# Kernel optimization log

Measured on AMD Instinct MI355X. Metric: run time of the kernel, lower is better.

## Reference

```python
import jax, jax.numpy as jnp
import numpy as np

R_EPS = 1e-15

def _sdf_net(x, W1, b1, W2, b2):
    h = jax.nn.relu(x @ W1 + b1)
    return h @ W2 + b2  # [..., 1+feat]

def _fd_gradient(x, W1, b1, W2, b2, eps):
    # central finite differences of the SDF along the 3 axes
    offs = eps * jnp.eye(3, dtype=x.dtype)              # [3,3]
    xp = x[None, :, :] + offs[:, None, :]               # [3,P,3]
    xm = x[None, :, :] - offs[:, None, :]
    sp = _sdf_net(xp, W1, b1, W2, b2)[..., 0]           # [3,P]
    sm = _sdf_net(xm, W1, b1, W2, b2)[..., 0]
    return ((sp - sm) / (2.0 * eps)).T                  # [P,3]

def _softplus100(x):
    # torch.nn.Softplus(beta=100)
    return jax.nn.softplus(100.0 * x) / 100.0

def _exclusive_cumprod(a):
    ones = jnp.ones_like(a[:, :1])
    return jnp.cumprod(jnp.concatenate([ones, a], -1), -1)[:, :-1]

def _sample_pdf(bins, weights, n_samples):
    # bins [R,K], weights [R,K-1]; deterministic inverse-CDF sampling (det=True)
    weights = weights + 1e-5
    pdf = weights / jnp.sum(weights, -1, keepdims=True)
    cdf = jnp.cumsum(pdf, -1)
    cdf = jnp.concatenate([jnp.zeros_like(cdf[:, :1]), cdf], -1)  # [R,K]
    K = cdf.shape[-1]
    u = jnp.linspace(0.5 / n_samples, 1.0 - 0.5 / n_samples, n_samples, dtype=bins.dtype)
    u = jnp.broadcast_to(u[None], (bins.shape[0], n_samples))
    inds = jax.vmap(lambda c, uu: jnp.searchsorted(c, uu, side='right'))(cdf, u)
    below = jnp.clip(inds - 1, 0, K - 1)
    above = jnp.clip(inds, 0, K - 1)
    cdf_b = jnp.take_along_axis(cdf, below, -1)
    cdf_a = jnp.take_along_axis(cdf, above, -1)
    bin_b = jnp.take_along_axis(bins, below, -1)
    bin_a = jnp.take_along_axis(bins, above, -1)
    denom = cdf_a - cdf_b
    denom = jnp.where(denom < 1e-5, jnp.ones_like(denom), denom)
    t = (u - cdf_b) / denom
    return bin_b + t * (bin_a - bin_b)

def _forward(rays_o, rays_d, W1, b1, W2, b2, Wc1, bc1, Wc2, bc2, inv_s_param,
             num_steps, upsample_steps, bound):
    B, N = rays_o.shape[:2]
    ro = rays_o.reshape(-1, 3)
    rd = rays_d.reshape(-1, 3)
    R = ro.shape[0]
    bnd = float(bound)
    # near/far from cube bound
    tmin = (-bnd - ro) / (rd + R_EPS)
    tmax = (bnd - ro) / (rd + R_EPS)
    near = jnp.max(jnp.minimum(tmin, tmax), -1, keepdims=True)
    far = jnp.min(jnp.maximum(tmin, tmax), -1, keepdims=True)
    near = jnp.maximum(near, 0.05)
    z = jnp.linspace(0.0, 1.0, num_steps, dtype=ro.dtype)[None]
    z_vals = near + (far - near) * z                     # [R,S0]
    sample_dist = (far - near) / num_steps               # [R,1]
    pts = ro[:, None, :] + rd[:, None, :] * z_vals[..., None]
    pts = jnp.clip(pts, -bnd, bnd)
    # --- coarse SDF pass + inverse-CDF importance resampling (torch.no_grad) ---
    sdf_c = _sdf_net(pts.reshape(-1, 3), W1, b1, W2, b2)[:, 0].reshape(R, num_steps)
    sdf_c = jax.lax.stop_gradient(sdf_c)
    d_c = z_vals[:, 1:] - z_vals[:, :-1]
    mid_sdf = 0.5 * (sdf_c[:, 1:] + sdf_c[:, :-1])
    cos_val = jnp.clip((sdf_c[:, 1:] - sdf_c[:, :-1]) / (d_c + 1e-5), -1e3, 0.0)
    prev_c = jax.nn.sigmoid((mid_sdf - cos_val * d_c * 0.5) * 64.0)
    next_c = jax.nn.sigmoid((mid_sdf + cos_val * d_c * 0.5) * 64.0)
    alpha_c = jnp.clip((prev_c - next_c + 1e-5) / (prev_c + 1e-5), 0.0, 1.0)
    w_c = alpha_c * _exclusive_cumprod(1.0 - alpha_c + 1e-7)
    new_z = jax.lax.stop_gradient(_sample_pdf(z_vals, w_c, upsample_steps))
    z_vals = jnp.sort(jnp.concatenate([z_vals, new_z], -1), -1)
    S = num_steps + upsample_steps
    # --- fine pass: deltas / midpoints / shading / NeuS compositing ---
    deltas = z_vals[:, 1:] - z_vals[:, :-1]
    deltas = jnp.concatenate([deltas, jnp.broadcast_to(sample_dist, (R, 1))], -1)
    z_mid = jnp.concatenate([z_vals[:, :-1] + 0.5 * deltas[:, :-1], z_vals[:, -1:]], -1)
    new_pts = ro[:, None, :] + rd[:, None, :] * z_mid[..., None]
    new_pts = jnp.clip(new_pts, -bnd, bnd)
    flat_pts = new_pts.reshape(-1, 3)                    # [R*S,3]
    out = _sdf_net(flat_pts, W1, b1, W2, b2)
    sdf = out[:, :1]
    feat = out[:, 1:]
    grad = _fd_gradient(flat_pts, W1, b1, W2, b2, 0.005)  # eps=0.005*(1-ratio), ratio=0
    normal = grad / (1e-5 + jnp.linalg.norm(grad, axis=-1, keepdims=True))
    dirs = jnp.broadcast_to(rd[:, None, :], new_pts.shape).reshape(-1, 3)
    cin = jnp.concatenate([flat_pts, dirs, normal, feat], -1)
    color = jax.nn.sigmoid(jax.nn.relu(cin @ Wc1 + bc1) @ Wc2 + bc2)   # [R*S,3]
    inv_s = jnp.exp(10.0 * inv_s_param)                   # forward_variance()
    true_cos = jnp.sum(dirs * normal, -1, keepdims=True)
    iter_cos = -_softplus100(-true_cos)                   # cos_anneal_ratio = 1.0
    d_flat = deltas.reshape(-1, 1)
    prev_cdf = jax.nn.sigmoid((sdf - iter_cos * d_flat * 0.5) * inv_s)
    next_cdf = jax.nn.sigmoid((sdf + iter_cos * d_flat * 0.5) * inv_s)
    alpha = jnp.clip((prev_cdf - next_cdf + 1e-5) / (prev_cdf + 1e-5), 0.0, 1.0).reshape(R, S)
    weights = alpha * _exclusive_cumprod(1.0 - alpha + 1e-7)
    weights_sum = jnp.sum(weights, -1, keepdims=True)
    image = jnp.sum(color.reshape(R, S, 3) * weights[..., None], 1)
    image = image + (1.0 - weights_sum) * 1.0             # bg_color = 1
    return image.reshape(B, N, 3)

def setup_inputs() -> dict:
    key = jax.random.key(0)
    ks = jax.random.split(key, 8)
    B, N, H, F = 1, 4096, 64, 64
    rays_o = (jax.random.uniform(ks[0], (B, N, 3), jnp.float32) - 0.5) * 0.5
    d = jax.random.normal(ks[1], (B, N, 3), jnp.float32)
    rays_d = d / (1e-8 + jnp.linalg.norm(d, axis=-1, keepdims=True))
    def lin(k, i, o):
        return jax.random.normal(k, (i, o), jnp.float32) / np.sqrt(i).astype(np.float32)
    W1 = lin(ks[2], 3, H); b1 = jnp.zeros((H,), jnp.float32)
    W2 = lin(ks[3], H, 1 + F); b2 = jnp.zeros((1 + F,), jnp.float32)
    Wc1 = lin(ks[4], 9 + F, H); bc1 = jnp.zeros((H,), jnp.float32)
    Wc2 = lin(ks[5], H, 3); bc2 = jnp.zeros((3,), jnp.float32)
    inv_s_param = jnp.full((1,), 0.3, jnp.float32)
    return {"rays_o": rays_o, "rays_d": rays_d, "W1": W1, "b1": b1, "W2": W2, "b2": b2,
            "Wc1": Wc1, "bc1": bc1, "Wc2": Wc2, "bc2": bc2, "inv_s_param": inv_s_param,
            "num_steps": 64, "upsample_steps": 64, "bound": 1}

def reference(rays_o, rays_d, W1, b1, W2, b2, Wc1, bc1, Wc2, bc2, inv_s_param,
              num_steps, upsample_steps, bound):
    return _forward(rays_o, rays_d, W1, b1, W2, b2, Wc1, bc1, Wc2, bc2, inv_s_param,
                    num_steps, upsample_steps, bound)
```

## Files before the change

### kernel.cpp

```cpp
#include <hip/hip_runtime.h>
#include <hip/hip_bf16.h>
#include <cmath>

#define KS 84

#define OFF_W1    0
#define OFF_W1E   256
#define OFF_W1S   512
#define OFF_WC2   768
#define OFF_BC2   1024
#define OFF_GC    1028
#define OFF_AF    1032

typedef __attribute__((ext_vector_type(4))) short  short4v;
typedef __attribute__((ext_vector_type(8))) short  short8v;
typedef __attribute__((ext_vector_type(16))) float f32x16;

__device__ __forceinline__ float sigm(float x){ return 1.0f/(1.0f + expf(-x)); }
__device__ __forceinline__ float clampf(float x, float lo, float hi){ return fminf(fmaxf(x, lo), hi); }
__device__ __forceinline__ unsigned short f2bf(float x){
  __hip_bfloat16 h = __float2bfloat16(x);
  return *reinterpret_cast<unsigned short*>(&h);
}
__device__ __forceinline__ unsigned pk2(float a, float b){
  return (unsigned)f2bf(a) | ((unsigned)f2bf(b) << 16);
}
__device__ __forceinline__ unsigned cvt_pk_bf16(float a, float b){
  unsigned r;
  asm("v_cvt_pk_bf16_f32 %0, %1, %2" : "=v"(r) : "v"(a), "v"(b));
  return r;
}
__device__ __forceinline__ short8v lds_load8(const unsigned short* p){
  short4v lo = *(const short4v*)p;
  short4v hi = *(const short4v*)(p + 4);
  short8v r;
  r[0]=lo[0]; r[1]=lo[1]; r[2]=lo[2]; r[3]=lo[3];
  r[4]=hi[0]; r[5]=hi[1]; r[6]=hi[2]; r[7]=hi[3];
  return r;
}

__global__ __launch_bounds__(256)
void prep_weights(const float* __restrict__ W1, const float* __restrict__ b1,
                  const float* __restrict__ W2, const float* __restrict__ b2,
                  const float* __restrict__ Wc1, const float* __restrict__ bc1,
                  const float* __restrict__ Wc2, const float* __restrict__ bc2,
                  float* __restrict__ ws)
{
  __shared__ float LW2[4160];
  __shared__ float LWc1[4672];
  __shared__ float LW1[192];
  __shared__ float Lb1[64];
  __shared__ float Lb2[65];
  __shared__ float Lbc1[64];
  __shared__ float LWc2[192];
  __shared__ float Lbc2[3];
  __shared__ float s_cb[4][64];
  __shared__ unsigned short W2T[64*KS];
  __shared__ unsigned short ABUF[64*KS];
  const int tid  = threadIdx.x;
  const int lane = tid & 63;
  const int wv   = tid >> 6;
  const int l31  = lane & 31;
  const int h    = lane >> 5;

  {
    const float4* s4 = (const float4*)W2;
    float4* d4 = (float4*)LW2;
    for (int i = tid; i < 1040; i += 256) d4[i] = s4[i];
    const float4* c4 = (const float4*)Wc1;
    float4* e4 = (float4*)LWc1;
    for (int i = tid; i < 1168; i += 256) e4[i] = c4[i];
  }
  if (tid < 192) LW1[tid]  = W1[tid];
  if (tid < 64)  Lb1[tid]  = b1[tid];
  if (tid < 65)  Lb2[tid]  = b2[tid];
  if (tid < 64)  Lbc1[tid] = bc1[tid];
  if (tid < 192) LWc2[tid] = Wc2[tid];
  if (tid < 3)   Lbc2[tid] = bc2[tid];
  __syncthreads();

  for (int i = tid; i < 4096; i += 256){
    int k = i >> 6, t = i & 63;
    W2T[k*KS + t] = f2bf(LW2[k*65 + 1 + t]);
  }
  for (int i = tid; i < 576; i += 256){
    int ii = i >> 6, c = i & 63;
    ABUF[c*KS + 64 + ii] = f2bf(LWc1[ii*64 + c]);
  }
  for (int i = tid; i < 384; i += 256){
    int z = i >> 6, c = i & 63;
    ABUF[c*KS + 74 + z] = 0;
  }
  {
    int c = tid & 63, q = tid >> 6;
    float acc = 0.f;
    #pragma unroll
    for (int t = 16*q; t < 16*q + 16; ++t)
      acc = fmaf(Lb2[1+t], LWc1[(9+t)*64 + c], acc);
    s_cb[q][c] = acc;
  }
  if (tid < 64){
    int j = tid;
    float wx = LW1[j], wy = LW1[64+j], wz = LW1[128+j];
    float w2 = LW2[j*65];
    float Hx = 0.005f * fabsf(wx);
    float Hy = 0.005f * fabsf(wy);
    float Hz = 0.005f * fabsf(wz);
    float Sx = (wx < 0.f) ? -w2 : w2;
    float Sy = (wy < 0.f) ? -w2 : w2;
    float Sz = (wz < 0.f) ? -w2 : w2;
    ws[OFF_W1 + 4*j + 0] = wx;
    ws[OFF_W1 + 4*j + 1] = wy;
    ws[OFF_W1 + 4*j + 2] = wz;
    ws[OFF_W1 + 4*j + 3] = Lb1[j];
    ws[OFF_W1E + 4*j + 0] = Hx;
    ws[OFF_W1E + 4*j + 1] = Hy;
    ws[OFF_W1E + 4*j + 2] = Hz;
    ws[OFF_W1E + 4*j + 3] = w2;
    ws[OFF_W1S + 4*j + 0] = Sx;
    ws[OFF_W1S + 4*j + 1] = Sy;
    ws[OFF_W1S + 4*j + 2] = Sz;
    ws[OFF_W1S + 4*j + 3] = 0.f;
    float sx = Sx*Hx, sy = Sy*Hy, sz = Sz*Hz;
    #pragma unroll
    for (int off = 1; off < 64; off <<= 1){
      sx += __shfl_xor(sx, off);
      sy += __shfl_xor(sy, off);
      sz += __shfl_xor(sz, off);
    }
    if (j == 0){
      ws[OFF_GC + 0] = sx;
      ws[OFF_GC + 1] = sy;
      ws[OFF_GC + 2] = sz;
    }
  } else if (tid < 128){
    int j = tid - 64;
    ws[OFF_WC2 + 4*j + 0] = LWc2[j*3+0];
    ws[OFF_WC2 + 4*j + 1] = LWc2[j*3+1];
    ws[OFF_WC2 + 4*j + 2] = LWc2[j*3+2];
    ws[OFF_WC2 + 4*j + 3] = 0.f;
  } else if (tid < 132){
    int j = tid - 128;
    ws[OFF_BC2 + j] = (j < 3) ? Lbc2[j] : Lb2[0];
  }
  __syncthreads();

  if (tid < 64){
    float acc = Lbc1[tid] + ((s_cb[0][tid] + s_cb[1][tid]) + (s_cb[2][tid] + s_cb[3][tid]));
    ABUF[tid*KS + 73] = f2bf(acc);
  }
  {
    const int mb = wv & 1, kb = wv >> 1;
    f32x16 e;
    #pragma unroll
    for (int i = 0; i < 16; ++i) e[i] = 0.f;
    #pragma unroll
    for (int s = 0; s < 4; ++s){
      short8v afr;
      #pragma unroll
      for (int j = 0; j < 8; ++j)
        afr[j] = (short)f2bf(LWc1[(9 + 16*s + 8*h + j)*64 + 32*mb + l31]);
      short8v bfr = lds_load8(&W2T[(32*kb + l31)*KS + 16*s + 8*h]);
      e = __builtin_amdgcn_mfma_f32_32x32x16_bf16(afr, bfr, e, 0, 0, 0);
    }
    const int kcol = 32*kb + l31;
    #pragma unroll
    for (int r = 0; r < 16; ++r){
      int c = 32*mb + (r & 3) + 8*(r >> 2) + 4*h;
      ABUF[c*KS + kcol] = f2bf(e[r]);
    }
  }
  __syncthreads();

  for (int i = tid; i < 640; i += 256){
    int f = i >> 6, ln = i & 63;
    int mb = f / 5, kk = f - 5*mb;
    int c  = 32*mb + (ln & 31);
    int kb2 = 16*kk + 8*(ln >> 5);
    short8v v = lds_load8(&ABUF[c*KS + kb2]);
    *((short8v*)(((unsigned short*)(ws + OFF_AF)) + (size_t)i * 8)) = v;
  }
}

__global__ __launch_bounds__(128, 3)
void neus_render(const float* __restrict__ rays_o, const float* __restrict__ rays_d,
                 const float* __restrict__ inv_s_p, const float* __restrict__ ws,
                 float* __restrict__ out)
{
  __shared__ unsigned short s_aext[2][64*KS];
  __shared__ float4 s_wc2[64];
  __shared__ float  s_z[64];
  __shared__ float  s_cdf[64];
  __shared__ float  s_newz[64];
  __shared__ float  s_zall[128];
  __shared__ float  s_red[2][4];
  __shared__ float  s_wtot[2];

  const int tid  = threadIdx.x;
  const int lt   = tid;
  const int lane = tid & 63;
  const int wir  = tid >> 6;
  const int ray  = blockIdx.x;

  const float4* __restrict__ pW1  = (const float4*)(ws + OFF_W1);
  const float4* __restrict__ pW1E = (const float4*)(ws + OFF_W1E);
  const float4* __restrict__ pW1S = (const float4*)(ws + OFF_W1S);
  const float*  __restrict__ pbc2 = ws + OFF_BC2;
  const float*  __restrict__ pgc  = ws + OFF_GC;
  const float b20 = pbc2[3];

  if (tid < 64) s_wc2[tid] = ((const float4*)(ws + OFF_WC2))[tid];

  float ox = rays_o[ray*3], oy = rays_o[ray*3+1], oz = rays_o[ray*3+2];
  float dx = rays_d[ray*3], dy = rays_d[ray*3+1], dz = rays_d[ray*3+2];
  float tnx = (-1.f-ox)/(dx+1e-15f), tfx = (1.f-ox)/(dx+1e-15f);
  float tny = (-1.f-oy)/(dy+1e-15f), tfy = (1.f-oy)/(dy+1e-15f);
  float tnz = (-1.f-oz)/(dz+1e-15f), tfz = (1.f-oz)/(dz+1e-15f);
  float nearv = fmaxf(fmaxf(fminf(tnx,tfx), fminf(tny,tfy)), fminf(tnz,tfz));
  float farv  = fminf(fminf(fmaxf(tnx,tfx), fmaxf(tny,tfy)), fmaxf(tnz,tfz));
  nearv = fmaxf(nearv, 0.05f);
  const float sd = (farv - nearv) * (1.f/64.f);

  if (wir == 0){
    float zt = nearv + (farv-nearv) * ((float)lane * (1.f/63.f));
    float px = clampf(ox + dx*zt, -1.f, 1.f);
    float py = clampf(oy + dy*zt, -1.f, 1.f);
    float pz = clampf(oz + dz*zt, -1.f, 1.f);
    float acc0 = b20, acc1 = 0.f;
    #pragma unroll 4
    for (int q = 0; q < 32; ++q){
      int j = 2*q;
      float4 wa = pW1[j];
      float4 wb = pW1[j+1];
      float ea = pW1E[j].w;
      float eb = pW1E[j+1].w;
      float ha = fmaxf(fmaf(px, wa.x, fmaf(py, wa.y, fmaf(pz, wa.z, wa.w))), 0.f);
      float hb = fmaxf(fmaf(px, wb.x, fmaf(py, wb.y, fmaf(pz, wb.z, wb.w))), 0.f);
      acc0 = fmaf(ha, ea, acc0);
      acc1 = fmaf(hb, eb, acc1);
    }
    float acc = acc0 + acc1;
    s_z[lane] = zt;
    float s1  = __shfl_down(acc, 1);
    float zt1 = nearv + (farv-nearv) * ((float)(lane+1) * (1.f/63.f));
    float a_c = 0.f, qv = 1.f;
    if (lane < 63){
      float dc   = zt1 - zt;
      float mid  = 0.5f*(acc + s1);
      float cosv = clampf((s1-acc)/(dc+1e-5f), -1000.f, 0.f);
      float est  = cosv*dc*0.5f;
      float pcv  = sigm((mid-est)*64.f);
      float ncv  = sigm((mid+est)*64.f);
      a_c = clampf((pcv-ncv+1e-5f)/(pcv+1e-5f), 0.f, 1.f);
      qv  = 1.f - a_c + 1e-7f;
    }
    float p = qv;
    #pragma unroll
    for (int off = 1; off < 64; off <<= 1){
      float t = __shfl_up(p, off);
      if (lane >= off) p *= t;
    }
    float ec = __shfl_up(p, 1);
    if (lane == 0) ec = 1.f;
    float wvv = (lane < 63) ? (a_c*ec + 1e-5f) : 0.f;
    float tot = wvv;
    #pragma unroll
    for (int off = 32; off > 0; off >>= 1) tot += __shfl_xor(tot, off);
    float cs = wvv;
    #pragma unroll
    for (int off = 1; off < 64; off <<= 1){
      float t = __shfl_up(cs, off);
      if (lane >= off) cs += t;
    }
    if (lane == 0)  s_cdf[0] = 0.f;
    if (lane < 63)  s_cdf[lane+1] = cs / tot;
  }
  __syncthreads();

  if (wir == 0){
    float u = ((float)lane + 0.5f) * (1.f/64.f);
    int lo = 0, hi = 64;
    while (lo < hi){
      int m = (lo+hi) >> 1;
      if (s_cdf[m] <= u) lo = m+1; else hi = m;
    }
    int below = lo - 1;
    int above = lo < 63 ? lo : 63;
    float cb = s_cdf[below], ca = s_cdf[above];
    float bb = s_z[below],   ba = s_z[above];
    float den = ca - cb; if (den < 1e-5f) den = 1.f;
    float tt = (u - cb)/den;
    s_newz[lane] = bb + tt*(ba - bb);
  }
  __syncthreads();

  const short8v* pAF = (const short8v*)(ws + OFF_AF);
  short8v af[10];
  #pragma unroll
  for (int f = 0; f < 10; ++f) af[f] = pAF[f*64 + lane];

  {
    float v; int pos;
    if (lt < 64){
      v = s_z[lt];
      int lo = 0, hi = 64;
      while (lo < hi){ int m=(lo+hi)>>1; if (s_newz[m] < v) lo = m+1; else hi = m; }
      pos = lt + lo;
    } else {
      int jj = lt - 64;
      v = s_newz[jj];
      int lo = 0, hi = 64;
      while (lo < hi){ int m=(lo+hi)>>1; if (s_z[m] <= v) lo = m+1; else hi = m; }
      pos = jj + lo;
    }
    s_zall[pos] = v;
  }
  __syncthreads();

  float zc = s_zall[lt];
  float zn = s_zall[lt < 127 ? lt+1 : 127];
  float delta = (lt < 127) ? (zn - zc) : sd;
  float zm    = (lt < 127) ? (zc + 0.5f*delta) : zc;
  float px = clampf(ox + dx*zm, -1.f, 1.f);
  float py = clampf(oy + dy*zm, -1.f, 1.f);
  float pz = clampf(oz + dz*zm, -1.f, 1.f);

  unsigned short* arow = &s_aext[wir][(unsigned)lane * KS];
  float sa0 = b20, sa1 = 0.f;
  float gxa = pgc[0], gya = pgc[1], gza = pgc[2];
  float gxb = 0.f, gyb = 0.f, gzb = 0.f;
  #pragma unroll 2
  for (int q = 0; q < 16; ++q){
    int j = 4*q;
    float4 w0 = pW1[j],   e0 = pW1E[j],   s0 = pW1S[j];
    float4 w1 = pW1[j+1], e1 = pW1E[j+1], s1v = pW1S[j+1];
    float4 w2 = pW1[j+2], e2 = pW1E[j+2], s2v = pW1S[j+2];
    float4 w3 = pW1[j+3], e3 = pW1E[j+3], s3v = pW1S[j+3];
    float base0 = fmaf(px, w0.x, fmaf(py, w0.y, fmaf(pz, w0.z, w0.w)));
    float base1 = fmaf(px, w1.x, fmaf(py, w1.y, fmaf(pz, w1.z, w1.w)));
    float base2 = fmaf(px, w2.x, fmaf(py, w2.y, fmaf(pz, w2.z, w2.w)));
    float base3 = fmaf(px, w3.x, fmaf(py, w3.y, fmaf(pz, w3.z, w3.w)));
    float hv0 = fmaxf(base0, 0.f), hv1 = fmaxf(base1, 0.f);
    float hv2 = fmaxf(base2, 0.f), hv3 = fmaxf(base3, 0.f);
    sa0 = fmaf(hv0, e0.w, sa0); sa0 = fmaf(hv1, e1.w, sa0);
    sa1 = fmaf(hv2, e2.w, sa1); sa1 = fmaf(hv3, e3.w, sa1);
    gxa = fmaf(__builtin_amdgcn_fmed3f(base0, -e0.x, e0.x), s0.x, gxa);
    gya = fmaf(__builtin_amdgcn_fmed3f(base0, -e0.y, e0.y), s0.y, gya);
    gza = fmaf(__builtin_amdgcn_fmed3f(base0, -e0.z, e0.z), s0.z, gza);
    gxa = fmaf(__builtin_amdgcn_fmed3f(base1, -e1.x, e1.x), s1v.x, gxa);
    gya = fmaf(__builtin_amdgcn_fmed3f(base1, -e1.y, e1.y), s1v.y, gya);
    gza = fmaf(__builtin_amdgcn_fmed3f(base1, -e1.z, e1.z), s1v.z, gza);
    gxb = fmaf(__builtin_amdgcn_fmed3f(base2, -e2.x, e2.x), s2v.x, gxb);
    gyb = fmaf(__builtin_amdgcn_fmed3f(base2, -e2.y, e2.y), s2v.y, gyb);
    gzb = fmaf(__builtin_amdgcn_fmed3f(base2, -e2.z, e2.z), s2v.z, gzb);
    gxb = fmaf(__builtin_amdgcn_fmed3f(base3, -e3.x, e3.x), s3v.x, gxb);
    gyb = fmaf(__builtin_amdgcn_fmed3f(base3, -e3.y, e3.y), s3v.y, gyb);
    gzb = fmaf(__builtin_amdgcn_fmed3f(base3, -e3.z, e3.z), s3v.z, gzb);
    *(unsigned*)&arow[j]   = cvt_pk_bf16(hv0, hv1);
    *(unsigned*)&arow[j+2] = cvt_pk_bf16(hv2, hv3);
  }
  float sdfv = sa0 + sa1;
  float gx = (gxa+gxb)*100.f, gy = (gya+gyb)*100.f, gz = (gza+gzb)*100.f;
  float gn = 1e-5f + sqrtf(gx*gx + gy*gy + gz*gz);
  float nx = gx/gn, ny = gy/gn, nz = gz/gn;

  *(unsigned*)&arow[64] = cvt_pk_bf16(px, py);
  *(unsigned*)&arow[66] = cvt_pk_bf16(pz, dx);
  *(unsigned*)&arow[68] = cvt_pk_bf16(dy, dz);
  *(unsigned*)&arow[70] = cvt_pk_bf16(nx, ny);
  *(unsigned*)&arow[72] = cvt_pk_bf16(nz, 1.0f);
  *(unsigned*)&arow[74] = 0u;
  *(unsigned*)&arow[76] = 0u;
  *(unsigned*)&arow[78] = 0u;

  const float inv_s = expf(10.f * inv_s_p[0]);
  float tcos = dx*nx + dy*ny + dz*nz;
  float aarg = -100.f * tcos;
  float spv  = (aarg > 0.f) ? (aarg + log1pf(expf(-aarg))) : log1pf(expf(aarg));
  float iter_cos = -(spv * 0.01f);
  float est = iter_cos * delta * 0.5f;
  float pcv = sigm((sdfv - est)*inv_s);
  float ncv = sigm((sdfv + est)*inv_s);
  float alpha = clampf((pcv - ncv + 1e-5f)/(pcv + 1e-5f), 0.f, 1.f);

  float qv = 1.f - alpha + 1e-7f;
  float p = qv;
  #pragma unroll
  for (int off = 1; off < 64; off <<= 1){
    float t = __shfl_up(p, off);
    if (lane >= off) p *= t;
  }
  if (lane == 63) s_wtot[wir] = p;
  __syncthreads();
  float excl = __shfl_up(p, 1);
  if (lane == 0) excl = 1.f;
  if (wir == 1) excl *= s_wtot[0];
  float w  = alpha * excl;

  f32x16 acc00, acc01, acc10, acc11;
  #pragma unroll
  for (int i = 0; i < 16; ++i){ acc00[i]=0.f; acc01[i]=0.f; acc10[i]=0.f; acc11[i]=0.f; }
  const unsigned short* aw = s_aext[wir];
  const int scol = lane & 31;
  const int half8 = (lane >> 5) * 8;
  #pragma unroll
  for (int kk = 0; kk < 5; ++kk){
    int koff = 16*kk + half8;
    short8v b0 = lds_load8(&aw[ scol      * KS + koff]);
    short8v b1 = lds_load8(&aw[(32+scol) * KS + koff]);
    acc00 = __builtin_amdgcn_mfma_f32_32x32x16_bf16(af[kk],   b0, acc00, 0, 0, 0);
    acc10 = __builtin_amdgcn_mfma_f32_32x32x16_bf16(af[5+kk], b0, acc10, 0, 0, 0);
    acc01 = __builtin_amdgcn_mfma_f32_32x32x16_bf16(af[kk],   b1, acc01, 0, 0, 0);
    acc11 = __builtin_amdgcn_mfma_f32_32x32x16_bf16(af[5+kk], b1, acc11, 0, 0, 0);
  }

  float pr0=0.f,pr1=0.f,pr2=0.f,pr3=0.f,pr4=0.f,pr5=0.f;
  const int halfoff = (lane >> 5) * 4;
  #pragma unroll
  for (int r = 0; r < 16; ++r){
    int ci = (r & 3) + 8*(r >> 2) + halfoff;
    float4 wA = s_wc2[ci];
    float4 wB = s_wc2[32 + ci];
    float v;
    v = fmaxf(acc00[r], 0.f); pr0 = fmaf(v, wA.x, pr0); pr1 = fmaf(v, wA.y, pr1); pr2 = fmaf(v, wA.z, pr2);
    v = fmaxf(acc10[r], 0.f); pr0 = fmaf(v, wB.x, pr0); pr1 = fmaf(v, wB.y, pr1); pr2 = fmaf(v, wB.z, pr2);
    v = fmaxf(acc01[r], 0.f); pr3 = fmaf(v, wA.x, pr3); pr4 = fmaf(v, wA.y, pr4); pr5 = fmaf(v, wA.z, pr5);
    v = fmaxf(acc11[r], 0.f); pr3 = fmaf(v, wB.x, pr3); pr4 = fmaf(v, wB.y, pr4); pr5 = fmaf(v, wB.z, pr5);
  }
  pr0 += __shfl_xor(pr0, 32); pr1 += __shfl_xor(pr1, 32); pr2 += __shfl_xor(pr2, 32);
  pr3 += __shfl_xor(pr3, 32); pr4 += __shfl_xor(pr4, 32); pr5 += __shfl_xor(pr5, 32);
  const bool hihalf = (lane >= 32);
  float c0 = sigm((hihalf ? pr3 : pr0) + pbc2[0]);
  float c1 = sigm((hihalf ? pr4 : pr1) + pbc2[1]);
  float c2 = sigm((hihalf ? pr5 : pr2) + pbc2[2]);

  float r0 = w, r1 = w*c0, r2 = w*c1, r3 = w*c2;
  #pragma unroll
  for (int off = 32; off > 0; off >>= 1){
    r0 += __shfl_xor(r0, off);
    r1 += __shfl_xor(r1, off);
    r2 += __shfl_xor(r2, off);
    r3 += __shfl_xor(r3, off);
  }
  if (lane == 0){
    s_red[wir][0]=r0; s_red[wir][1]=r1; s_red[wir][2]=r2; s_red[wir][3]=r3;
  }
  __syncthreads();
  if (tid == 0){
    float wsum = s_red[0][0] + s_red[1][0];
    float bg = 1.f - wsum;
    out[ray*3+0] = s_red[0][1] + s_red[1][1] + bg;
    out[ray*3+1] = s_red[0][2] + s_red[1][2] + bg;
    out[ray*3+2] = s_red[0][3] + s_red[1][3] + bg;
  }
}

extern "C" void kernel_launch(void* const* d_in, const int* in_sizes, int n_in,
                              void* d_out, int out_size, void* d_ws, size_t ws_size,
                              hipStream_t stream)
{
  const float* rays_o = (const float*)d_in[0];
  const float* rays_d = (const float*)d_in[1];
  const float* W1  = (const float*)d_in[2];
  const float* b1  = (const float*)d_in[3];
  const float* W2  = (const float*)d_in[4];
  const float* b2  = (const float*)d_in[5];
  const float* Wc1 = (const float*)d_in[6];
  const float* bc1 = (const float*)d_in[7];
  const float* Wc2 = (const float*)d_in[8];
  const float* bc2 = (const float*)d_in[9];
  const float* inv_s = (const float*)d_in[10];
  float* out = (float*)d_out;
  float* ws  = (float*)d_ws;

  prep_weights<<<1, 256, 0, stream>>>(W1, b1, W2, b2, Wc1, bc1, Wc2, bc2, ws);

  const int R = in_sizes[0] / 3;
  dim3 grid(R), block(128);
  neus_render<<<grid, block, 0, stream>>>(rays_o, rays_d, inv_s, ws, out);
}
```

Baseline: 126.3 us.

## Render each ray with a single wavefront looping over two sample halves

The render kernel now launches one 64-thread wavefront per ray instead of two. The single wave processes the 128 merged samples in two passes, carrying transmittance across passes in a register, and halves the LDS activation buffer. This removes the idle second wave during the coarse and sampling phases and the cross-wave shared-memory reductions, and it raises the occupancy target. In exchange the per-ray work is serialized inside one wave, which lengthens each ray's critical path.

```diff
diff --git a/kernel.cpp b/kernel.cpp
--- a/kernel.cpp
+++ b/kernel.cpp
@@ -21,9 +21,6 @@
 __device__ __forceinline__ unsigned short f2bf(float x){
   __hip_bfloat16 h = __float2bfloat16(x);
   return *reinterpret_cast<unsigned short*>(&h);
-}
-__device__ __forceinline__ unsigned pk2(float a, float b){
-  return (unsigned)f2bf(a) | ((unsigned)f2bf(b) << 16);
 }
 __device__ __forceinline__ unsigned cvt_pk_bf16(float a, float b){
   unsigned r;
@@ -182,24 +179,19 @@
   }
 }
 
-__global__ __launch_bounds__(128, 3)
+__global__ __launch_bounds__(64, 8)
 void neus_render(const float* __restrict__ rays_o, const float* __restrict__ rays_d,
                  const float* __restrict__ inv_s_p, const float* __restrict__ ws,
                  float* __restrict__ out)
 {
-  __shared__ unsigned short s_aext[2][64*KS];
+  __shared__ unsigned short s_aext[64*KS];
   __shared__ float4 s_wc2[64];
   __shared__ float  s_z[64];
   __shared__ float  s_cdf[64];
   __shared__ float  s_newz[64];
   __shared__ float  s_zall[128];
-  __shared__ float  s_red[2][4];
-  __shared__ float  s_wtot[2];
-
-  const int tid  = threadIdx.x;
-  const int lt   = tid;
-  const int lane = tid & 63;
-  const int wir  = tid >> 6;
+
+  const int lane = threadIdx.x;
   const int ray  = blockIdx.x;
 
   const float4* __restrict__ pW1  = (const float4*)(ws + OFF_W1);
@@ -209,10 +201,11 @@
   const float*  __restrict__ pgc  = ws + OFF_GC;
   const float b20 = pbc2[3];
 
-  if (tid < 64) s_wc2[tid] = ((const float4*)(ws + OFF_WC2))[tid];
+  s_wc2[lane] = ((const float4*)(ws + OFF_WC2))[lane];
 
   float ox = rays_o[ray*3], oy = rays_o[ray*3+1], oz = rays_o[ray*3+2];
   float dx = rays_d[ray*3], dy = rays_d[ray*3+1], dz = rays_d[ray*3+2];
+  const float inv_s = expf(10.f * inv_s_p[0]);
   float tnx = (-1.f-ox)/(dx+1e-15f), tfx = (1.f-ox)/(dx+1e-15f);
   float tny = (-1.f-oy)/(dy+1e-15f), tfy = (1.f-oy)/(dy+1e-15f);
   float tnz = (-1.f-oz)/(dz+1e-15f), tfz = (1.f-oz)/(dz+1e-15f);
@@ -221,7 +214,7 @@
   nearv = fmaxf(nearv, 0.05f);
   const float sd = (farv - nearv) * (1.f/64.f);
 
-  if (wir == 0){
+  {
     float zt = nearv + (farv-nearv) * ((float)lane * (1.f/63.f));
     float px = clampf(ox + dx*zt, -1.f, 1.f);
     float py = clampf(oy + dy*zt, -1.f, 1.f);
@@ -277,7 +270,7 @@
   }
   __syncthreads();
 
-  if (wir == 0){
+  {
     float u = ((float)lane + 0.5f) * (1.f/64.f);
     int lo = 0, hi = 64;
     while (lo < hi){
@@ -300,158 +293,157 @@
   for (int f = 0; f < 10; ++f) af[f] = pAF[f*64 + lane];
 
   {
-    float v; int pos;
-    if (lt < 64){
-      v = s_z[lt];
-      int lo = 0, hi = 64;
-      while (lo < hi){ int m=(lo+hi)>>1; if (s_newz[m] < v) lo = m+1; else hi = m; }
-      pos = lt + lo;
-    } else {
-      int jj = lt - 64;
-      v = s_newz[jj];
-      int lo = 0, hi = 64;
-      while (lo < hi){ int m=(lo+hi)>>1; if (s_z[m] <= v) lo = m+1; else hi = m; }
-      pos = jj + lo;
-    }
-    s_zall[pos] = v;
-  }
-  __syncthreads();
-
-  float zc = s_zall[lt];
-  float zn = s_zall[lt < 127 ? lt+1 : 127];
-  float delta = (lt < 127) ? (zn - zc) : sd;
-  float zm    = (lt < 127) ? (zc + 0.5f*delta) : zc;
-  float px = clampf(ox + dx*zm, -1.f, 1.f);
-  float py = clampf(oy + dy*zm, -1.f, 1.f);
-  float pz = clampf(oz + dz*zm, -1.f, 1.f);
-
-  unsigned short* arow = &s_aext[wir][(unsigned)lane * KS];
-  float sa0 = b20, sa1 = 0.f;
-  float gxa = pgc[0], gya = pgc[1], gza = pgc[2];
-  float gxb = 0.f, gyb = 0.f, gzb = 0.f;
-  #pragma unroll 2
-  for (int q = 0; q < 16; ++q){
-    int j = 4*q;
-    float4 w0 = pW1[j],   e0 = pW1E[j],   s0 = pW1S[j];
-    float4 w1 = pW1[j+1], e1 = pW1E[j+1], s1v = pW1S[j+1];
-    float4 w2 = pW1[j+2], e2 = pW1E[j+2], s2v = pW1S[j+2];
-    float4 w3 = pW1[j+3], e3 = pW1E[j+3], s3v = pW1S[j+3];
-    float base0 = fmaf(px, w0.x, fmaf(py, w0.y, fmaf(pz, w0.z, w0.w)));
-    float base1 = fmaf(px, w1.x, fmaf(py, w1.y, fmaf(pz, w1.z, w1.w)));
-    float base2 = fmaf(px, w2.x, fmaf(py, w2.y, fmaf(pz, w2.z, w2.w)));
-    float base3 = fmaf(px, w3.x, fmaf(py, w3.y, fmaf(pz, w3.z, w3.w)));
-    float hv0 = fmaxf(base0, 0.f), hv1 = fmaxf(base1, 0.f);
-    float hv2 = fmaxf(base2, 0.f), hv3 = fmaxf(base3, 0.f);
-    sa0 = fmaf(hv0, e0.w, sa0); sa0 = fmaf(hv1, e1.w, sa0);
-    sa1 = fmaf(hv2, e2.w, sa1); sa1 = fmaf(hv3, e3.w, sa1);
-    gxa = fmaf(__builtin_amdgcn_fmed3f(base0, -e0.x, e0.x), s0.x, gxa);
-    gya = fmaf(__builtin_amdgcn_fmed3f(base0, -e0.y, e0.y), s0.y, gya);
-    gza = fmaf(__builtin_amdgcn_fmed3f(base0, -e0.z, e0.z), s0.z, gza);
-    gxa = fmaf(__builtin_amdgcn_fmed3f(base1, -e1.x, e1.x), s1v.x, gxa);
-    gya = fmaf(__builtin_amdgcn_fmed3f(base1, -e1.y, e1.y), s1v.y, gya);
-    gza = fmaf(__builtin_amdgcn_fmed3f(base1, -e1.z, e1.z), s1v.z, gza);
-    gxb = fmaf(__builtin_amdgcn_fmed3f(base2, -e2.x, e2.x), s2v.x, gxb);
-    gyb = fmaf(__builtin_amdgcn_fmed3f(base2, -e2.y, e2.y), s2v.y, gyb);
-    gzb = fmaf(__builtin_amdgcn_fmed3f(base2, -e2.z, e2.z), s2v.z, gzb);
-    gxb = fmaf(__builtin_amdgcn_fmed3f(base3, -e3.x, e3.x), s3v.x, gxb);
-    gyb = fmaf(__builtin_amdgcn_fmed3f(base3, -e3.y, e3.y), s3v.y, gyb);
-    gzb = fmaf(__builtin_amdgcn_fmed3f(base3, -e3.z, e3.z), s3v.z, gzb);
-    *(unsigned*)&arow[j]   = cvt_pk_bf16(hv0, hv1);
-    *(unsigned*)&arow[j+2] = cvt_pk_bf16(hv2, hv3);
-  }
-  float sdfv = sa0 + sa1;
-  float gx = (gxa+gxb)*100.f, gy = (gya+gyb)*100.f, gz = (gza+gzb)*100.f;
-  float gn = 1e-5f + sqrtf(gx*gx + gy*gy + gz*gz);
-  float nx = gx/gn, ny = gy/gn, nz = gz/gn;
-
-  *(unsigned*)&arow[64] = cvt_pk_bf16(px, py);
-  *(unsigned*)&arow[66] = cvt_pk_bf16(pz, dx);
-  *(unsigned*)&arow[68] = cvt_pk_bf16(dy, dz);
-  *(unsigned*)&arow[70] = cvt_pk_bf16(nx, ny);
-  *(unsigned*)&arow[72] = cvt_pk_bf16(nz, 1.0f);
-  *(unsigned*)&arow[74] = 0u;
-  *(unsigned*)&arow[76] = 0u;
-  *(unsigned*)&arow[78] = 0u;
-
-  const float inv_s = expf(10.f * inv_s_p[0]);
-  float tcos = dx*nx + dy*ny + dz*nz;
-  float aarg = -100.f * tcos;
-  float spv  = (aarg > 0.f) ? (aarg + log1pf(expf(-aarg))) : log1pf(expf(aarg));
-  float iter_cos = -(spv * 0.01f);
-  float est = iter_cos * delta * 0.5f;
-  float pcv = sigm((sdfv - est)*inv_s);
-  float ncv = sigm((sdfv + est)*inv_s);
-  float alpha = clampf((pcv - ncv + 1e-5f)/(pcv + 1e-5f), 0.f, 1.f);
-
-  float qv = 1.f - alpha + 1e-7f;
-  float p = qv;
-  #pragma unroll
-  for (int off = 1; off < 64; off <<= 1){
-    float t = __shfl_up(p, off);
-    if (lane >= off) p *= t;
-  }
-  if (lane == 63) s_wtot[wir] = p;
-  __syncthreads();
-  float excl = __shfl_up(p, 1);
-  if (lane == 0) excl = 1.f;
-  if (wir == 1) excl *= s_wtot[0];
-  float w  = alpha * excl;
-
-  f32x16 acc00, acc01, acc10, acc11;
-  #pragma unroll
-  for (int i = 0; i < 16; ++i){ acc00[i]=0.f; acc01[i]=0.f; acc10[i]=0.f; acc11[i]=0.f; }
-  const unsigned short* aw = s_aext[wir];
+    float v0 = s_z[lane];
+    int lo0 = 0, hi0 = 64;
+    while (lo0 < hi0){ int m=(lo0+hi0)>>1; if (s_newz[m] < v0) lo0 = m+1; else hi0 = m; }
+    float v1 = s_newz[lane];
+    int lo1 = 0, hi1 = 64;
+    while (lo1 < hi1){ int m=(lo1+hi1)>>1; if (s_z[m] <= v1) lo1 = m+1; else hi1 = m; }
+    s_zall[lane + lo0] = v0;
+    s_zall[lane + lo1] = v1;
+  }
+  __syncthreads();
+
+  unsigned short* arow = &s_aext[(unsigned)lane * KS];
+  const unsigned short* aw = s_aext;
   const int scol = lane & 31;
   const int half8 = (lane >> 5) * 8;
-  #pragma unroll
-  for (int kk = 0; kk < 5; ++kk){
-    int koff = 16*kk + half8;
-    short8v b0 = lds_load8(&aw[ scol      * KS + koff]);
-    short8v b1 = lds_load8(&aw[(32+scol) * KS + koff]);
-    acc00 = __builtin_amdgcn_mfma_f32_32x32x16_bf16(af[kk],   b0, acc00, 0, 0, 0);
-    acc10 = __builtin_amdgcn_mfma_f32_32x32x16_bf16(af[5+kk], b0, acc10, 0, 0, 0);
-    acc01 = __builtin_amdgcn_mfma_f32_32x32x16_bf16(af[kk],   b1, acc01, 0, 0, 0);
-    acc11 = __builtin_amdgcn_mfma_f32_32x32x16_bf16(af[5+kk], b1, acc11, 0, 0, 0);
-  }
-
-  float pr0=0.f,pr1=0.f,pr2=0.f,pr3=0.f,pr4=0.f,pr5=0.f;
   const int halfoff = (lane >> 5) * 4;
-  #pragma unroll
-  for (int r = 0; r < 16; ++r){
-    int ci = (r & 3) + 8*(r >> 2) + halfoff;
-    float4 wA = s_wc2[ci];
-    float4 wB = s_wc2[32 + ci];
-    float v;
-    v = fmaxf(acc00[r], 0.f); pr0 = fmaf(v, wA.x, pr0); pr1 = fmaf(v, wA.y, pr1); pr2 = fmaf(v, wA.z, pr2);
-    v = fmaxf(acc10[r], 0.f); pr0 = fmaf(v, wB.x, pr0); pr1 = fmaf(v, wB.y, pr1); pr2 = fmaf(v, wB.z, pr2);
-    v = fmaxf(acc01[r], 0.f); pr3 = fmaf(v, wA.x, pr3); pr4 = fmaf(v, wA.y, pr4); pr5 = fmaf(v, wA.z, pr5);
-    v = fmaxf(acc11[r], 0.f); pr3 = fmaf(v, wB.x, pr3); pr4 = fmaf(v, wB.y, pr4); pr5 = fmaf(v, wB.z, pr5);
-  }
-  pr0 += __shfl_xor(pr0, 32); pr1 += __shfl_xor(pr1, 32); pr2 += __shfl_xor(pr2, 32);
-  pr3 += __shfl_xor(pr3, 32); pr4 += __shfl_xor(pr4, 32); pr5 += __shfl_xor(pr5, 32);
   const bool hihalf = (lane >= 32);
-  float c0 = sigm((hihalf ? pr3 : pr0) + pbc2[0]);
-  float c1 = sigm((hihalf ? pr4 : pr1) + pbc2[1]);
-  float c2 = sigm((hihalf ? pr5 : pr2) + pbc2[2]);
-
-  float r0 = w, r1 = w*c0, r2 = w*c1, r3 = w*c2;
+  const float gc0 = pgc[0], gc1 = pgc[1], gc2 = pgc[2];
+  float rA = 0.f, rB = 0.f, rC = 0.f, rD = 0.f;
+  float Tc = 1.f;
+
+  for (int b = 0; b < 2; ++b){
+    const int lt2 = 64*b + lane;
+    float zc = s_zall[lt2];
+    float zn = s_zall[lt2 < 127 ? lt2+1 : 127];
+    float delta = (lt2 < 127) ? (zn - zc) : sd;
+    float zm    = (lt2 < 127) ? (zc + 0.5f*delta) : zc;
+    float px = clampf(ox + dx*zm, -1.f, 1.f);
+    float py = clampf(oy + dy*zm, -1.f, 1.f);
+    float pz = clampf(oz + dz*zm, -1.f, 1.f);
+
+    float sa0 = b20, sa1 = 0.f;
+    float gxa = gc0, gya = gc1, gza = gc2;
+    float gxb = 0.f, gyb = 0.f, gzb = 0.f;
+    #pragma unroll 2
+    for (int q = 0; q < 16; ++q){
+      int j = 4*q;
+      float4 w0 = pW1[j],   e0 = pW1E[j],   s0 = pW1S[j];
+      float4 w1 = pW1[j+1], e1 = pW1E[j+1], s1v = pW1S[j+1];
+      float4 w2 = pW1[j+2], e2 = pW1E[j+2], s2v = pW1S[j+2];
+      float4 w3 = pW1[j+3], e3 = pW1E[j+3], s3v = pW1S[j+3];
+      float base0 = fmaf(px, w0.x, fmaf(py, w0.y, fmaf(pz, w0.z, w0.w)));
+      float base1 = fmaf(px, w1.x, fmaf(py, w1.y, fmaf(pz, w1.z, w1.w)));
+      float base2 = fmaf(px, w2.x, fmaf(py, w2.y, fmaf(pz, w2.z, w2.w)));
+      float base3 = fmaf(px, w3.x, fmaf(py, w3.y, fmaf(pz, w3.z, w3.w)));
+      float hv0 = fmaxf(base0, 0.f), hv1 = fmaxf(base1, 0.f);
+      float hv2 = fmaxf(base2, 0.f), hv3 = fmaxf(base3, 0.f);
+      sa0 = fmaf(hv0, e0.w, sa0); sa0 = fmaf(hv1, e1.w, sa0);
+      sa1 = fmaf(hv2, e2.w, sa1); sa1 = fmaf(hv3, e3.w, sa1);
+      gxa = fmaf(__builtin_amdgcn_fmed3f(base0, -e0.x, e0.x), s0.x, gxa);
+      gya = fmaf(__builtin_amdgcn_fmed3f(base0, -e0.y, e0.y), s0.y, gya);
+      gza = fmaf(__builtin_amdgcn_fmed3f(base0, -e0.z, e0.z), s0.z, gza);
+      gxa = fmaf(__builtin_amdgcn_fmed3f(base1, -e1.x, e1.x), s1v.x, gxa);
+      gya = fmaf(__builtin_amdgcn_fmed3f(base1, -e1.y, e1.y), s1v.y, gya);
+      gza = fmaf(__builtin_amdgcn_fmed3f(base1, -e1.z, e1.z), s1v.z, gza);
+      gxb = fmaf(__builtin_amdgcn_fmed3f(base2, -e2.x, e2.x), s2v.x, gxb);
+      gyb = fmaf(__builtin_amdgcn_fmed3f(base2, -e2.y, e2.y), s2v.y, gyb);
+      gzb = fmaf(__builtin_amdgcn_fmed3f(base2, -e2.z, e2.z), s2v.z, gzb);
+      gxb = fmaf(__builtin_amdgcn_fmed3f(base3, -e3.x, e3.x), s3v.x, gxb);
+      gyb = fmaf(__builtin_amdgcn_fmed3f(base3, -e3.y, e3.y), s3v.y, gyb);
+      gzb = fmaf(__builtin_amdgcn_fmed3f(base3, -e3.z, e3.z), s3v.z, gzb);
+      *(unsigned*)&arow[j]   = cvt_pk_bf16(hv0, hv1);
+      *(unsigned*)&arow[j+2] = cvt_pk_bf16(hv2, hv3);
+    }
+    float sdfv = sa0 + sa1;
+    float gx = (gxa+gxb)*100.f, gy = (gya+gyb)*100.f, gz = (gza+gzb)*100.f;
+    float gn = 1e-5f + sqrtf(gx*gx + gy*gy + gz*gz);
+    float nx = gx/gn, ny = gy/gn, nz = gz/gn;
+
+    *(unsigned*)&arow[64] = cvt_pk_bf16(px, py);
+    *(unsigned*)&arow[66] = cvt_pk_bf16(pz, dx);
+    *(unsigned*)&arow[68] = cvt_pk_bf16(dy, dz);
+    *(unsigned*)&arow[70] = cvt_pk_bf16(nx, ny);
+    *(unsigned*)&arow[72] = cvt_pk_bf16(nz, 1.0f);
+    *(unsigned*)&arow[74] = 0u;
+    *(unsigned*)&arow[76] = 0u;
+    *(unsigned*)&arow[78] = 0u;
+
+    float tcos = dx*nx + dy*ny + dz*nz;
+    float aarg = -100.f * tcos;
+    float spv  = (aarg > 0.f) ? (aarg + log1pf(expf(-aarg))) : log1pf(expf(aarg));
+    float iter_cos = -(spv * 0.01f);
+    float est = iter_cos * delta * 0.5f;
+    float pcv = sigm((sdfv - est)*inv_s);
+    float ncv = sigm((sdfv + est)*inv_s);
+    float alpha = clampf((pcv - ncv + 1e-5f)/(pcv + 1e-5f), 0.f, 1.f);
+
+    float qv = 1.f - alpha + 1e-7f;
+    float p = qv;
+    #pragma unroll
+    for (int off = 1; off < 64; off <<= 1){
+      float t = __shfl_up(p, off);
+      if (lane >= off) p *= t;
+    }
+    float excl = __shfl_up(p, 1);
+    if (lane == 0) excl = 1.f;
+    excl *= Tc;
+    float w = alpha * excl;
+    Tc *= __shfl(p, 63);
+
+    __syncthreads();
+
+    f32x16 acc00, acc01, acc10, acc11;
+    #pragma unroll
+    for (int i = 0; i < 16; ++i){ acc00[i]=0.f; acc01[i]=0.f; acc10[i]=0.f; acc11[i]=0.f; }
+    #pragma unroll
+    for (int kk = 0; kk < 5; ++kk){
+      int koff = 16*kk + half8;
+      short8v b0 = lds_load8(&aw[ scol      * KS + koff]);
+      short8v b1 = lds_load8(&aw[(32+scol) * KS + koff]);
+      acc00 = __builtin_amdgcn_mfma_f32_32x32x16_bf16(af[kk],   b0, acc00, 0, 0, 0);
+      acc10 = __builtin_amdgcn_mfma_f32_32x32x16_bf16(af[5+kk], b0, acc10, 0, 0, 0);
+      acc01 = __builtin_amdgcn_mfma_f32_32x32x16_bf16(af[kk],   b1, acc01, 0, 0, 0);
+      acc11 = __builtin_amdgcn_mfma_f32_32x32x16_bf16(af[5+kk], b1, acc11, 0, 0, 0);
+    }
+
+    float pr0=0.f,pr1=0.f,pr2=0.f,pr3=0.f,pr4=0.f,pr5=0.f;
+    #pragma unroll
+    for (int r = 0; r < 16; ++r){
+      int ci = (r & 3) + 8*(r >> 2) + halfoff;
+      float4 wA = s_wc2[ci];
+      float4 wB = s_wc2[32 + ci];
+      float v;
+      v = fmaxf(acc00[r], 0.f); pr0 = fmaf(v, wA.x, pr0); pr1 = fmaf(v, wA.y, pr1); pr2 = fmaf(v, wA.z, pr2);
+      v = fmaxf(acc10[r], 0.f); pr0 = fmaf(v, wB.x, pr0); pr1 = fmaf(v, wB.y, pr1); pr2 = fmaf(v, wB.z, pr2);
+      v = fmaxf(acc01[r], 0.f); pr3 = fmaf(v, wA.x, pr3); pr4 = fmaf(v, wA.y, pr4); pr5 = fmaf(v, wA.z, pr5);
+      v = fmaxf(acc11[r], 0.f); pr3 = fmaf(v, wB.x, pr3); pr4 = fmaf(v, wB.y, pr4); pr5 = fmaf(v, wB.z, pr5);
+    }
+    pr0 += __shfl_xor(pr0, 32); pr1 += __shfl_xor(pr1, 32); pr2 += __shfl_xor(pr2, 32);
+    pr3 += __shfl_xor(pr3, 32); pr4 += __shfl_xor(pr4, 32); pr5 += __shfl_xor(pr5, 32);
+    float c0 = sigm((hihalf ? pr3 : pr0) + pbc2[0]);
+    float c1 = sigm((hihalf ? pr4 : pr1) + pbc2[1]);
+    float c2 = sigm((hihalf ? pr5 : pr2) + pbc2[2]);
+
+    rA += w; rB += w*c0; rC += w*c1; rD += w*c2;
+
+    __syncthreads();
+  }
+
   #pragma unroll
   for (int off = 32; off > 0; off >>= 1){
-    r0 += __shfl_xor(r0, off);
-    r1 += __shfl_xor(r1, off);
-    r2 += __shfl_xor(r2, off);
-    r3 += __shfl_xor(r3, off);
+    rA += __shfl_xor(rA, off);
+    rB += __shfl_xor(rB, off);
+    rC += __shfl_xor(rC, off);
+    rD += __shfl_xor(rD, off);
   }
   if (lane == 0){
-    s_red[wir][0]=r0; s_red[wir][1]=r1; s_red[wir][2]=r2; s_red[wir][3]=r3;
-  }
-  __syncthreads();
-  if (tid == 0){
-    float wsum = s_red[0][0] + s_red[1][0];
-    float bg = 1.f - wsum;
-    out[ray*3+0] = s_red[0][1] + s_red[1][1] + bg;
-    out[ray*3+1] = s_red[0][2] + s_red[1][2] + bg;
-    out[ray*3+2] = s_red[0][3] + s_red[1][3] + bg;
+    float bg = 1.f - rA;
+    out[ray*3+0] = rB + bg;
+    out[ray*3+1] = rC + bg;
+    out[ray*3+2] = rD + bg;
   }
 }
 
@@ -476,6 +468,6 @@
   prep_weights<<<1, 256, 0, stream>>>(W1, b1, W2, b2, Wc1, bc1, Wc2, bc2, ws);
 
   const int R = in_sizes[0] / 3;
-  dim3 grid(R), block(128);
+  dim3 grid(R), block(64);
   neus_render<<<grid, block, 0, stream>>>(rays_o, rays_d, inv_s, ws, out);
 }
```

Measured after the change: 123.5 us (median of 3 runs). -2.2%, faster.
